# Optimization experiments

Measured on AMD Instinct MI355X. Metric: run time of the kernel, lower is better.

The kernel has to match this reference:

```python
import jax, jax.numpy as jnp
import numpy as np

N = 50000
E = 500000
C = 128
NUM_TYPES = 32
DIM_TOK = 94
STEPS = 3
BLOCKS = 2
NUM_ET = 3
LN_EPS = 1e-5


def setup_inputs() -> dict:
    key = jax.random.key(0)
    ks = jax.random.split(key, 16)
    s = 0.05
    return {
        "x_type": jax.random.randint(ks[0], (N,), 0, NUM_TYPES),
        "x_tok": jax.random.randint(ks[1], (N,), 0, DIM_TOK),
        "x_small": jax.random.normal(ks[2], (N, 2), jnp.float32),
        "edge_index": jax.random.randint(ks[3], (2, E), 0, N),
        "edge_type": jax.random.randint(ks[4], (E,), 0, NUM_ET),
        "conv_w": jax.random.normal(ks[5], (BLOCKS, NUM_ET, STEPS, C, C), jnp.float32) * s,
        "gru_wih": jax.random.normal(ks[6], (BLOCKS, NUM_ET, 3 * C, C), jnp.float32) * s,
        "gru_whh": jax.random.normal(ks[7], (BLOCKS, NUM_ET, 3 * C, C), jnp.float32) * s,
        "gru_bih": jnp.zeros((BLOCKS, NUM_ET, 3 * C), jnp.float32),
        "gru_bhh": jnp.zeros((BLOCKS, NUM_ET, 3 * C), jnp.float32),
        "ln_g": jnp.ones((BLOCKS, C), jnp.float32),
        "ln_b": jnp.zeros((BLOCKS, C), jnp.float32),
        "head_w1": jax.random.normal(ks[8], (C, C), jnp.float32) * s,
        "head_b1": jnp.zeros((C,), jnp.float32),
        "head_w2": jax.random.normal(ks[9], (2, C), jnp.float32) * s,
        "head_b2": jnp.zeros((2,), jnp.float32),
    }


def _gru_cell(x, h, wih, whh, bih, bhh):
    # torch.nn.GRUCell: gates ordered (r, z, n)
    gi = x @ wih.T + bih  # [N, 3C]
    gh = h @ whh.T + bhh
    gi_r, gi_z, gi_n = jnp.split(gi, 3, axis=-1)
    gh_r, gh_z, gh_n = jnp.split(gh, 3, axis=-1)
    r = jax.nn.sigmoid(gi_r + gh_r)
    z = jax.nn.sigmoid(gi_z + gh_z)
    n = jnp.tanh(gi_n + r * gh_n)
    return (1.0 - z) * n + z * h


def _forward(x_small, conv_w, gru_wih, gru_whh, gru_bih, gru_bhh, ln_g, ln_b,
             head_w1, head_b1, head_w2, head_b2, x_type, x_tok, edge_index, edge_type):
    # build_features: one-hot type, one-hot (clamped) token, small feats
    h_type = jax.nn.one_hot(x_type, NUM_TYPES, dtype=x_small.dtype)
    h_tok = jax.nn.one_hot(jnp.clip(x_tok, 0, DIM_TOK - 1), DIM_TOK, dtype=x_small.dtype)
    h = jnp.concatenate([h_type, h_tok, x_small], axis=1)  # [N, C]

    src, dst = edge_index[0], edge_index[1]

    for b in range(BLOCKS):
        total = jnp.zeros_like(h)
        for t in range(NUM_ET):
            # edge-type masking implemented as weighted scatter-add (sum aggr)
            em = (edge_type == t).astype(h.dtype)[:, None]  # [E, 1]
            m = h
            for s in range(STEPS):
                x = m @ conv_w[b, t, s]                     # [N, C]
                agg = jax.ops.segment_sum(x[src] * em, dst, num_segments=N)
                m = _gru_cell(agg, m,
                              gru_wih[b, t], gru_whh[b, t],
                              gru_bih[b, t], gru_bhh[b, t])
            total = total + m
        # LayerNorm(residual) + ReLU; dropout=0 (eval)
        hr = h + total
        mu = jnp.mean(hr, axis=-1, keepdims=True)
        var = jnp.var(hr, axis=-1, keepdims=True)
        h = (hr - mu) * jax.lax.rsqrt(var + LN_EPS) * ln_g[b] + ln_b[b]
        h = jax.nn.relu(h)

    # head applied per-node (module returns head(h), not head(pooled))
    z = jax.nn.relu(h @ head_w1.T + head_b1)
    return z @ head_w2.T + head_b2  # [N, 2]


def reference(x_type, x_tok, x_small, edge_index, edge_type, conv_w, gru_wih, gru_whh,
              gru_bih, gru_bhh, ln_g, ln_b, head_w1, head_b1, head_w2, head_b2):
    return _forward(x_small, conv_w, gru_wih, gru_whh, gru_bih, gru_bhh, ln_g, ln_b,
                    head_w1, head_b1, head_w2, head_b2, x_type, x_tok, edge_index, edge_type)
```

## Files before the change

kernel.cpp:

```cpp
#include <hip/hip_runtime.h>
#include <cstdint>
#include <cstddef>

#define N_NODES 50000
#define N_EDGES 500000
#define NB 782
#define NT 150000
#define NCHUNK2 586
#define FS 49152
#define PSTR 136
#define MAXOFF 12799744u

typedef _Float16 half8 __attribute__((ext_vector_type(8)));
typedef _Float16 half2v __attribute__((ext_vector_type(2)));
typedef float floatx4 __attribute__((ext_vector_type(4)));

__device__ __forceinline__ float sigmoid_(float x) { return 1.f / (1.f + __expf(-x)); }
__device__ __forceinline__ float tanh_(float x) {
  float t = __expf(-2.f * fabsf(x));
  float r = (1.f - t) / (1.f + t);
  return copysignf(r, x);
}

__global__ __launch_bounds__(256) void k_features(_Float16* __restrict__ h,
    const int* __restrict__ xtype, const int* __restrict__ xtok,
    const float* __restrict__ xs) {
  int idx = blockIdx.x * 256 + threadIdx.x;
  if (idx >= N_NODES * 128) return;
  int n = idx >> 7, c = idx & 127;
  float v;
  if (c < 32) {
    v = (xtype[n] == c) ? 1.f : 0.f;
  } else if (c < 126) {
    int tk = xtok[n];
    tk = tk < 0 ? 0 : (tk > 93 ? 93 : tk);
    v = (tk == (c - 32)) ? 1.f : 0.f;
  } else {
    v = xs[n * 2 + (c - 126)];
  }
  h[idx] = (_Float16)v;
}

__global__ __launch_bounds__(256) void k_hist(const int* __restrict__ ei,
    const int* __restrict__ et, int* __restrict__ counts) {
  int e = blockIdx.x * 256 + threadIdx.x;
  if (e >= N_EDGES) return;
  int d = ei[N_EDGES + e];
  int ty = et[e] & 3;
  if ((unsigned)d < N_NODES && ty < 3) atomicAdd(&counts[ty * N_NODES + d], 1);
}

__global__ __launch_bounds__(256) void k_scan_a(const int* __restrict__ counts,
    int* __restrict__ bsum) {
  int i = blockIdx.x * 256 + threadIdx.x;
  int v = (i < NT) ? counts[i] : 0;
  int lane = threadIdx.x & 63, wv = threadIdx.x >> 6;
#pragma unroll
  for (int off = 32; off > 0; off >>= 1) v += __shfl_xor(v, off);
  __shared__ int ws[4];
  if (lane == 0) ws[wv] = v;
  __syncthreads();
  if (threadIdx.x == 0) bsum[blockIdx.x] = ws[0] + ws[1] + ws[2] + ws[3];
}

__global__ __launch_bounds__(256) void k_scan_b(const int* __restrict__ bsum,
    int* __restrict__ boff) {
  __shared__ int ws[4];
  __shared__ int run_s;
  if (threadIdx.x == 0) run_s = 0;
  __syncthreads();
  int lane = threadIdx.x & 63, wv = threadIdx.x >> 6;
  for (int base = 0; base < NCHUNK2; base += 256) {
    int i = base + threadIdx.x;
    int v = (i < NCHUNK2) ? bsum[i] : 0;
    int s = v;
#pragma unroll
    for (int off = 1; off < 64; off <<= 1) { int u = __shfl_up(s, off); if (lane >= off) s += u; }
    if (lane == 63) ws[wv] = s;
    __syncthreads();
    int woff = 0;
#pragma unroll
    for (int w = 0; w < 4; ++w) woff += (w < wv) ? ws[w] : 0;
    int run = run_s;
    if (i < NCHUNK2) boff[i] = run + woff + s - v;
    __syncthreads();
    if (threadIdx.x == 255) run_s = run + woff + s;
    __syncthreads();
  }
  if (threadIdx.x == 0) boff[NCHUNK2] = run_s;
}

__global__ __launch_bounds__(256) void k_scan_c(const int* __restrict__ counts,
    const int* __restrict__ boff, int* __restrict__ ptr, int* __restrict__ fill) {
  int i = blockIdx.x * 256 + threadIdx.x;
  int v = (i < NT) ? counts[i] : 0;
  int lane = threadIdx.x & 63, wv = threadIdx.x >> 6;
  int s = v;
#pragma unroll
  for (int off = 1; off < 64; off <<= 1) { int u = __shfl_up(s, off); if (lane >= off) s += u; }
  __shared__ int ws[4];
  if (lane == 63) ws[wv] = s;
  __syncthreads();
  int woff = 0;
#pragma unroll
  for (int w = 0; w < 4; ++w) woff += (w < wv) ? ws[w] : 0;
  int excl = boff[blockIdx.x] + woff + s - v;
  if (i < NT) { ptr[i] = excl; fill[i] = excl; }
  if (blockIdx.x == 0 && threadIdx.x == 0) ptr[NT] = boff[NCHUNK2];
}

__global__ __launch_bounds__(256) void k_place(const int* __restrict__ ei,
    const int* __restrict__ et, int* __restrict__ fill, int* __restrict__ csr) {
  int e = blockIdx.x * 256 + threadIdx.x;
  if (e >= N_EDGES) return;
  int srcv = ei[e], d = ei[N_EDGES + e], ty = et[e] & 3;
  if ((unsigned)d >= N_NODES || (unsigned)srcv >= N_NODES || ty >= 3) return;
  int pos = atomicAdd(&fill[ty * N_NODES + d], 1);
  if ((unsigned)pos < N_EDGES) csr[pos] = srcv << 8;
}

#define PREP_A (18 * 4 * 24 * 512)
#define PREP_B (6 * 4 * 24 * 512)
__global__ __launch_bounds__(256) void k_prep_all(const float* __restrict__ cw,
    const float* __restrict__ wih, const float* __restrict__ whh,
    const float* __restrict__ hw1, _Float16* __restrict__ dcomb,
    _Float16* __restrict__ dwhh, _Float16* __restrict__ dw1) {
  int idx0 = blockIdx.x * 256 + threadIdx.x;
  if (idx0 < PREP_A) {
    int idx = idx0;
    int j = idx & 7, lane = (idx >> 3) & 63;
    int r = idx >> 9;
    int ct = r % 24;
    int r2 = r / 24;
    int kc = r2 & 3, mat = r2 >> 2;
    int bt = mat / 3;
    int k = kc * 32 + ((lane >> 4) & 3) * 8 + j;
    int n = ct * 16 + (lane & 15);
    const float* wrow = cw + ((size_t)mat * 128 + k) * 128;
    const float* irow = wih + ((size_t)bt * 384 + n) * 128;
    float acc = 0.f;
#pragma unroll
    for (int q = 0; q < 128; q += 4) {
      floatx4 a = *(const floatx4*)(wrow + q);
      floatx4 b = *(const floatx4*)(irow + q);
      acc += a[0] * b[0] + a[1] * b[1] + a[2] * b[2] + a[3] * b[3];
    }
    dcomb[idx] = (_Float16)acc;
  } else if (idx0 < PREP_A + PREP_B) {
    int idx = idx0 - PREP_A;
    int j = idx & 7, lane = (idx >> 3) & 63;
    int r = idx >> 9;
    int ct = r % 24;
    int r2 = r / 24;
    int kc = r2 & 3, bt = r2 >> 2;
    int k = kc * 32 + ((lane >> 4) & 3) * 8 + j;
    int n = ct * 16 + (lane & 15);
    dwhh[idx] = (_Float16)whh[((size_t)bt * 384 + n) * 128 + k];
  } else if (idx0 < PREP_A + PREP_B + 16384) {
    int idx = idx0 - PREP_A - PREP_B;
    int j = idx & 7, lane = (idx >> 3) & 63, ct = (idx >> 9) & 7, kc = (idx >> 12) & 3;
    int k = kc * 32 + ((lane >> 4) & 3) * 8 + j;
    int n = ct * 16 + (lane & 15);
    dw1[idx] = (_Float16)hw1[n * 128 + k];
  }
}

__global__ __launch_bounds__(512, 4) void k_step(
    const _Float16* __restrict__ Mbase, const size_t mstride,
    _Float16* __restrict__ Sout,
    const int* __restrict__ ptr, const int* __restrict__ csr,
    const _Float16* __restrict__ WPC, const _Float16* __restrict__ WHH,
    const float* __restrict__ bi2, const float* __restrict__ bh2) {
  __shared__ __attribute__((aligned(16))) _Float16 Plds[64 * PSTR];
  __shared__ __attribute__((aligned(16))) _Float16 Mlds[64 * PSTR];
  int bid = blockIdx.x;
  int t = bid / NB, blk = bid - t * NB;
  int tid = threadIdx.x;
  int wave = tid >> 6, lane = tid & 63;
  int quad = lane >> 4, l16 = lane & 15;
  int rowbase = blk * 64;
  const size_t NC = (size_t)N_NODES * 128;
  const _Float16* Mp = Mbase + mstride * t;
  const char* Mb = (const char*)Mp;
  _Float16* Sp = Sout + (size_t)t * NC;

#pragma unroll
  for (int it = 0; it < 2; ++it) {
    int r = it * 32 + (tid >> 4);
    int c = (tid & 15) * 8;
    int gr = rowbase + r; if (gr >= N_NODES) gr = N_NODES - 1;
    half8 v = *(const half8*)(Mp + (size_t)gr * 128 + c);
    *(half8*)(&Mlds[r * PSTR + c]) = v;
  }

  const int* ptrT = ptr + t * N_NODES;
  int g = quad;
  int coff = l16 * 16;
  int nlA = wave * 8 + g, nlB = nlA + 4;
  int nA = rowbase + nlA, nB = rowbase + nlB;
  int iA = 0, eA = 0, iB = 0, eB = 0;
  if (nA < N_NODES) { iA = ptrT[nA]; eA = ptrT[nA + 1]; }
  if (nB < N_NODES) { iB = ptrT[nB]; eB = ptrT[nB + 1]; }
  if (iA < 0) iA = 0; if (eA > N_EDGES) eA = N_EDGES;
  if (iB < 0) iB = 0; if (eB > N_EDGES) eB = N_EDGES;
  half8 accA = {}, accB = {};
  for (;;) {
    bool a0 = iA < eA, a1 = iA + 1 < eA;
    bool c0 = iB < eB, c1 = iB + 1 < eB;
    if (!__any(a0 || c0)) break;
    if (a0) {
      unsigned off = (unsigned)csr[iA];
      if (off > MAXOFF) off = 0;
      accA += *(const half8*)(Mb + off + coff);
    }
    if (c0) {
      unsigned off = (unsigned)csr[iB];
      if (off > MAXOFF) off = 0;
      accB += *(const half8*)(Mb + off + coff);
    }
    if (a1) {
      unsigned off = (unsigned)csr[iA + 1];
      if (off > MAXOFF) off = 0;
      accA += *(const half8*)(Mb + off + coff);
    }
    if (c1) {
      unsigned off = (unsigned)csr[iB + 1];
      if (off > MAXOFF) off = 0;
      accB += *(const half8*)(Mb + off + coff);
    }
    iA += 2; iB += 2;
  }
  *(half8*)(&Plds[nlA * PSTR + l16 * 8]) = accA;
  *(half8*)(&Plds[nlB * PSTR + l16 * 8]) = accB;
  __syncthreads();

  const half8* wpc = (const half8*)(WPC + (size_t)t * 3 * FS);
  const half8* whh = (const half8*)(WHH + (size_t)t * FS);
  const float* bi = bi2 + (size_t)t * 384;
  const float* bh = bh2 + (size_t)t * 384;
  int u = wave;
  floatx4 zero = {0.f, 0.f, 0.f, 0.f};
  floatx4 aR[4], aZ[4], aNP[4], aNM[4];
#pragma unroll
  for (int rt = 0; rt < 4; ++rt) { aR[rt] = zero; aZ[rt] = zero; aNP[rt] = zero; aNM[rt] = zero; }
#pragma unroll
  for (int kc = 0; kc < 4; ++kc) {
    half8 af[4];
#pragma unroll
    for (int rt = 0; rt < 4; ++rt)
      af[rt] = *(const half8*)(&Plds[(rt * 16 + l16) * PSTR + kc * 32 + quad * 8]);
    half8 br = wpc[(kc * 24 + u) * 64 + lane];
    half8 bz = wpc[(kc * 24 + 8 + u) * 64 + lane];
    half8 bn = wpc[(kc * 24 + 16 + u) * 64 + lane];
#pragma unroll
    for (int rt = 0; rt < 4; ++rt) {
      aR[rt] = __builtin_amdgcn_mfma_f32_16x16x32_f16(af[rt], br, aR[rt], 0, 0, 0);
      aZ[rt] = __builtin_amdgcn_mfma_f32_16x16x32_f16(af[rt], bz, aZ[rt], 0, 0, 0);
      aNP[rt] = __builtin_amdgcn_mfma_f32_16x16x32_f16(af[rt], bn, aNP[rt], 0, 0, 0);
    }
  }
#pragma unroll
  for (int kc = 0; kc < 4; ++kc) {
    half8 af[4];
#pragma unroll
    for (int rt = 0; rt < 4; ++rt)
      af[rt] = *(const half8*)(&Mlds[(rt * 16 + l16) * PSTR + kc * 32 + quad * 8]);
    half8 br = whh[(kc * 24 + u) * 64 + lane];
    half8 bz = whh[(kc * 24 + 8 + u) * 64 + lane];
    half8 bn = whh[(kc * 24 + 16 + u) * 64 + lane];
#pragma unroll
    for (int rt = 0; rt < 4; ++rt) {
      aR[rt] = __builtin_amdgcn_mfma_f32_16x16x32_f16(af[rt], br, aR[rt], 0, 0, 0);
      aZ[rt] = __builtin_amdgcn_mfma_f32_16x16x32_f16(af[rt], bz, aZ[rt], 0, 0, 0);
      aNM[rt] = __builtin_amdgcn_mfma_f32_16x16x32_f16(af[rt], bn, aNM[rt], 0, 0, 0);
    }
  }
  int col = u * 16 + l16;
  float br_ = bi[col] + bh[col];
  float bz_ = bi[128 + col] + bh[128 + col];
  float bin = bi[256 + col], bhn = bh[256 + col];
#pragma unroll
  for (int rt = 0; rt < 4; ++rt) {
#pragma unroll
    for (int q = 0; q < 4; ++q) {
      int lr = rt * 16 + quad * 4 + q;
      int row = rowbase + lr;
      if (row < N_NODES) {
        float r = sigmoid_(aR[rt][q] + br_);
        float z = sigmoid_(aZ[rt][q] + bz_);
        float nt = tanh_(aNP[rt][q] + bin + r * (aNM[rt][q] + bhn));
        float hold = (float)Mlds[lr * PSTR + col];
        Sp[(size_t)row * 128 + col] = (_Float16)((1.f - z) * nt + z * hold);
      }
    }
  }
}

__global__ __launch_bounds__(256) void k_ln(_Float16* __restrict__ h,
    const _Float16* __restrict__ S, const float* __restrict__ gamma,
    const float* __restrict__ beta) {
  int wave = threadIdx.x >> 6, lane = threadIdx.x & 63;
  int n = blockIdx.x * 4 + wave;
  if (n >= N_NODES) return;
  const size_t NC = (size_t)N_NODES * 128;
  size_t base = (size_t)n * 128 + lane * 2;
  half2v hv = *(const half2v*)(h + base);
  half2v s0 = *(const half2v*)(S + base);
  half2v s1 = *(const half2v*)(S + NC + base);
  half2v s2 = *(const half2v*)(S + 2 * NC + base);
  float v0 = (float)hv[0] + (float)s0[0] + (float)s1[0] + (float)s2[0];
  float v1 = (float)hv[1] + (float)s0[1] + (float)s1[1] + (float)s2[1];
  float s = v0 + v1, sq = v0 * v0 + v1 * v1;
#pragma unroll
  for (int off = 32; off > 0; off >>= 1) {
    s += __shfl_xor(s, off);
    sq += __shfl_xor(sq, off);
  }
  float mu = s * 0.0078125f;
  float var = sq * 0.0078125f - mu * mu;
  float rs = rsqrtf(var + 1e-5f);
  float o0 = (v0 - mu) * rs * gamma[lane * 2] + beta[lane * 2];
  float o1 = (v1 - mu) * rs * gamma[lane * 2 + 1] + beta[lane * 2 + 1];
  half2v ov; ov[0] = (_Float16)fmaxf(o0, 0.f); ov[1] = (_Float16)fmaxf(o1, 0.f);
  *(half2v*)(h + base) = ov;
}

__global__ __launch_bounds__(256, 4) void k_head(const _Float16* __restrict__ A,
    const _Float16* __restrict__ Wf, const float* __restrict__ bias,
    const float* __restrict__ w2, const float* __restrict__ b2,
    float* __restrict__ out) {
  __shared__ __attribute__((aligned(16))) _Float16 zl[64 * PSTR];
  __shared__ float w2s[256];
  int blk = blockIdx.x;
  int wave = threadIdx.x >> 6, lane = threadIdx.x & 63;
  int quad = lane >> 4, l16 = lane & 15;
  int rowbase = blk * 64;
  if (threadIdx.x < 256) w2s[threadIdx.x] = w2[threadIdx.x];
  const half8* wf = (const half8*)Wf;
  int ar[4];
#pragma unroll
  for (int rt = 0; rt < 4; ++rt) {
    int r = rowbase + rt * 16 + l16;
    ar[rt] = r < N_NODES ? r : N_NODES - 1;
  }
  floatx4 zero = {0.f, 0.f, 0.f, 0.f};
  floatx4 acc[4][2];
#pragma unroll
  for (int rt = 0; rt < 4; ++rt) { acc[rt][0] = zero; acc[rt][1] = zero; }
#pragma unroll
  for (int kc = 0; kc < 4; ++kc) {
    half8 af[4];
#pragma unroll
    for (int rt = 0; rt < 4; ++rt)
      af[rt] = *(const half8*)(A + (size_t)ar[rt] * 128 + kc * 32 + quad * 8);
    half8 b0 = wf[(kc * 8 + 2 * wave) * 64 + lane];
    half8 b1 = wf[(kc * 8 + 2 * wave + 1) * 64 + lane];
#pragma unroll
    for (int rt = 0; rt < 4; ++rt) {
      acc[rt][0] = __builtin_amdgcn_mfma_f32_16x16x32_f16(af[rt], b0, acc[rt][0], 0, 0, 0);
      acc[rt][1] = __builtin_amdgcn_mfma_f32_16x16x32_f16(af[rt], b1, acc[rt][1], 0, 0, 0);
    }
  }
  int col = wave * 32 + l16;
#pragma unroll
  for (int rt = 0; rt < 4; ++rt) {
#pragma unroll
    for (int q = 0; q < 4; ++q) {
      int lr = rt * 16 + quad * 4 + q;
      zl[lr * PSTR + col] = (_Float16)fmaxf(acc[rt][0][q] + bias[col], 0.f);
      zl[lr * PSTR + col + 16] = (_Float16)fmaxf(acc[rt][1][q] + bias[col + 16], 0.f);
    }
  }
  __syncthreads();
  int tid = threadIdx.x;
  if (tid < 128) {
    int lr = tid >> 1, o = tid & 1;
    int row = rowbase + lr;
    if (row < N_NODES) {
      const float* wr = w2s + o * 128;
      float a = 0.f;
#pragma unroll
      for (int k = 0; k < 128; ++k) a += (float)zl[lr * PSTR + k] * wr[k];
      out[(size_t)row * 2 + o] = a + b2[o];
    }
  }
}

extern "C" void kernel_launch(void* const* d_in, const int* in_sizes, int n_in,
                              void* d_out, int out_size, void* d_ws, size_t ws_size,
                              hipStream_t stream) {
  const int*   x_type  = (const int*)d_in[0];
  const int*   x_tok   = (const int*)d_in[1];
  const float* x_small = (const float*)d_in[2];
  const int*   eidx    = (const int*)d_in[3];
  const int*   etype   = (const int*)d_in[4];
  const float* conv_w  = (const float*)d_in[5];
  const float* gwih    = (const float*)d_in[6];
  const float* gwhh    = (const float*)d_in[7];
  const float* gbih    = (const float*)d_in[8];
  const float* gbhh    = (const float*)d_in[9];
  const float* ln_g    = (const float*)d_in[10];
  const float* ln_b    = (const float*)d_in[11];
  const float* hw1     = (const float*)d_in[12];
  const float* hb1     = (const float*)d_in[13];
  const float* hw2     = (const float*)d_in[14];
  const float* hb2     = (const float*)d_in[15];
  float* out = (float*)d_out;

  const size_t NC = (size_t)N_NODES * 128;
  char* W = (char*)d_ws;
  size_t off = 0;
  _Float16* h16 = (_Float16*)(W + off);     off += NC * 2;
  _Float16* S0  = (_Float16*)(W + off);     off += 3 * NC * 2;
  _Float16* S1  = (_Float16*)(W + off);     off += 3 * NC * 2;
  int* counts = (int*)(W + off);            off += (size_t)NT * 4;
  int* ptrv   = (int*)(W + off);            off += (size_t)(NT + 1) * 4;
  int* fill   = (int*)(W + off);            off += (size_t)NT * 4;
  int* bsum   = (int*)(W + off);            off += (NCHUNK2 + 1) * 4;
  int* boff   = (int*)(W + off);            off += (NCHUNK2 + 1) * 4;
  int* csr    = (int*)(W + off);            off += (size_t)N_EDGES * 4;
  _Float16* WPC = (_Float16*)(W + off);     off += (size_t)18 * FS * 2;
  _Float16* WHH = (_Float16*)(W + off);     off += (size_t)6 * FS * 2;
  _Float16* W1F = (_Float16*)(W + off);     off += (size_t)16384 * 2;

  k_features<<<(N_NODES * 128 + 255) / 256, 256, 0, stream>>>(h16, x_type, x_tok, x_small);
  hipMemsetAsync(counts, 0, (size_t)NT * 4, stream);
  k_hist<<<(N_EDGES + 255) / 256, 256, 0, stream>>>(eidx, etype, counts);
  k_scan_a<<<NCHUNK2, 256, 0, stream>>>(counts, bsum);
  k_scan_b<<<1, 256, 0, stream>>>(bsum, boff);
  k_scan_c<<<NCHUNK2, 256, 0, stream>>>(counts, boff, ptrv, fill);
  k_place<<<(N_EDGES + 255) / 256, 256, 0, stream>>>(eidx, etype, fill, csr);
  k_prep_all<<<(PREP_A + PREP_B + 16384 + 255) / 256, 256, 0, stream>>>(
      conv_w, gwih, gwhh, hw1, WPC, WHH, W1F);

  for (int b = 0; b < 2; ++b) {
    for (int s = 0; s < 3; ++s) {
      const _Float16* Msrc = (s == 0) ? h16 : ((s == 1) ? S0 : S1);
      size_t mstr = (s == 0) ? 0 : NC;
      _Float16* Sout = (s == 1) ? S1 : S0;
      k_step<<<3 * NB, 512, 0, stream>>>(Msrc, mstr, Sout, ptrv, csr,
          WPC + (size_t)(b * 9 + s) * FS, WHH + (size_t)b * 3 * FS,
          gbih + (size_t)b * 3 * 384, gbhh + (size_t)b * 3 * 384);
    }
    k_ln<<<(N_NODES + 3) / 4, 256, 0, stream>>>(h16, S0, ln_g + b * 128, ln_b + b * 128);
  }
  k_head<<<NB, 256, 0, stream>>>(h16, W1F, hb1, hw2, hb2, out);
}
```

Measured before the change: 825.7 us.

## Stage per-block CSR edge lists in LDS and compute combined weights with MFMA

The step kernel now loads the block's 65 row pointers and up to 768 edge source offsets into shared memory once, then gathers neighbor rows using LDS-resident indices with a 4-way unrolled loop, falling back to global reads past the cap. The combined conv_w·W_ih weight preparation moves from a scalar per-element dot-product kernel to an MFMA-based kernel, and the remaining prep goes into a separate kernel. This aims to cut repeated global index loads and the cost of weight preprocessing. The trade-offs are extra shared memory and synchronizations per block, plus fp16 rounding of the inputs before the combined weight product.

```diff
diff --git a/kernel.cpp b/kernel.cpp
--- a/kernel.cpp
+++ b/kernel.cpp
@@ -10,6 +10,7 @@
 #define FS 49152
 #define PSTR 136
 #define MAXOFF 12799744u
+#define ECAP 768
 
 typedef _Float16 half8 __attribute__((ext_vector_type(8)));
 typedef _Float16 half2v __attribute__((ext_vector_type(2)));
@@ -119,35 +120,70 @@
   if ((unsigned)pos < N_EDGES) csr[pos] = srcv << 8;
 }
 
-#define PREP_A (18 * 4 * 24 * 512)
+
+__global__ __launch_bounds__(512) void k_prep_cmb(const float* __restrict__ cw,
+    const float* __restrict__ wih, _Float16* __restrict__ dst) {
+  int mat = blockIdx.x >> 1, half = blockIdx.x & 1;
+  int bt = mat / 3;
+  int u = threadIdx.x >> 6, lane = threadIdx.x & 63;
+  int quad = lane >> 4, l16 = lane & 15;
+  floatx4 zero = {0.f, 0.f, 0.f, 0.f};
+  floatx4 acc[4][3];
+#pragma unroll
+  for (int rt = 0; rt < 4; ++rt)
+#pragma unroll
+    for (int cc = 0; cc < 3; ++cc) acc[rt][cc] = zero;
+#pragma unroll
+  for (int jc = 0; jc < 4; ++jc) {
+    half8 af[4], bf[3];
+#pragma unroll
+    for (int rt = 0; rt < 4; ++rt) {
+      int m = half * 64 + rt * 16 + l16;
+      const float* ap = cw + ((size_t)mat * 128 + m) * 128 + jc * 32 + quad * 8;
+      floatx4 a0 = *(const floatx4*)ap;
+      floatx4 a1 = *(const floatx4*)(ap + 4);
+#pragma unroll
+      for (int i = 0; i < 4; ++i) { af[rt][i] = (_Float16)a0[i]; af[rt][4 + i] = (_Float16)a1[i]; }
+    }
+#pragma unroll
+    for (int cc = 0; cc < 3; ++cc) {
+      int n = (u * 3 + cc) * 16 + l16;
+      const float* bp = wih + ((size_t)bt * 384 + n) * 128 + jc * 32 + quad * 8;
+      floatx4 b0 = *(const floatx4*)bp;
+      floatx4 b1 = *(const floatx4*)(bp + 4);
+#pragma unroll
+      for (int i = 0; i < 4; ++i) { bf[cc][i] = (_Float16)b0[i]; bf[cc][4 + i] = (_Float16)b1[i]; }
+    }
+#pragma unroll
+    for (int rt = 0; rt < 4; ++rt)
+#pragma unroll
+      for (int cc = 0; cc < 3; ++cc)
+        acc[rt][cc] = __builtin_amdgcn_mfma_f32_16x16x32_f16(af[rt], bf[cc], acc[rt][cc], 0, 0, 0);
+  }
+#pragma unroll
+  for (int rt = 0; rt < 4; ++rt) {
+#pragma unroll
+    for (int cc = 0; cc < 3; ++cc) {
+      int ctg = u * 3 + cc;
+#pragma unroll
+      for (int q = 0; q < 4; ++q) {
+        int k = half * 64 + rt * 16 + quad * 4 + q;
+        int kc2 = k >> 5, r5 = k & 31;
+        int lane2 = (r5 >> 3) * 16 + l16, j2 = r5 & 7;
+        dst[(size_t)mat * FS + (size_t)((kc2 * 24 + ctg) * 64 + lane2) * 8 + j2] =
+            (_Float16)acc[rt][cc][q];
+      }
+    }
+  }
+}
+
 #define PREP_B (6 * 4 * 24 * 512)
-__global__ __launch_bounds__(256) void k_prep_all(const float* __restrict__ cw,
-    const float* __restrict__ wih, const float* __restrict__ whh,
-    const float* __restrict__ hw1, _Float16* __restrict__ dcomb,
-    _Float16* __restrict__ dwhh, _Float16* __restrict__ dw1) {
+__global__ __launch_bounds__(256) void k_prep_misc(const float* __restrict__ whh,
+    const float* __restrict__ hw1, _Float16* __restrict__ dwhh,
+    _Float16* __restrict__ dw1) {
   int idx0 = blockIdx.x * 256 + threadIdx.x;
-  if (idx0 < PREP_A) {
+  if (idx0 < PREP_B) {
     int idx = idx0;
-    int j = idx & 7, lane = (idx >> 3) & 63;
-    int r = idx >> 9;
-    int ct = r % 24;
-    int r2 = r / 24;
-    int kc = r2 & 3, mat = r2 >> 2;
-    int bt = mat / 3;
-    int k = kc * 32 + ((lane >> 4) & 3) * 8 + j;
-    int n = ct * 16 + (lane & 15);
-    const float* wrow = cw + ((size_t)mat * 128 + k) * 128;
-    const float* irow = wih + ((size_t)bt * 384 + n) * 128;
-    float acc = 0.f;
-#pragma unroll
-    for (int q = 0; q < 128; q += 4) {
-      floatx4 a = *(const floatx4*)(wrow + q);
-      floatx4 b = *(const floatx4*)(irow + q);
-      acc += a[0] * b[0] + a[1] * b[1] + a[2] * b[2] + a[3] * b[3];
-    }
-    dcomb[idx] = (_Float16)acc;
-  } else if (idx0 < PREP_A + PREP_B) {
-    int idx = idx0 - PREP_A;
     int j = idx & 7, lane = (idx >> 3) & 63;
     int r = idx >> 9;
     int ct = r % 24;
@@ -156,8 +192,8 @@
     int k = kc * 32 + ((lane >> 4) & 3) * 8 + j;
     int n = ct * 16 + (lane & 15);
     dwhh[idx] = (_Float16)whh[((size_t)bt * 384 + n) * 128 + k];
-  } else if (idx0 < PREP_A + PREP_B + 16384) {
-    int idx = idx0 - PREP_A - PREP_B;
+  } else if (idx0 < PREP_B + 16384) {
+    int idx = idx0 - PREP_B;
     int j = idx & 7, lane = (idx >> 3) & 63, ct = (idx >> 9) & 7, kc = (idx >> 12) & 3;
     int k = kc * 32 + ((lane >> 4) & 3) * 8 + j;
     int n = ct * 16 + (lane & 15);
@@ -173,6 +209,8 @@
     const float* __restrict__ bi2, const float* __restrict__ bh2) {
   __shared__ __attribute__((aligned(16))) _Float16 Plds[64 * PSTR];
   __shared__ __attribute__((aligned(16))) _Float16 Mlds[64 * PSTR];
+  __shared__ int Elds[ECAP];
+  __shared__ int Pt[65];
   int bid = blockIdx.x;
   int t = bid / NB, blk = bid - t * NB;
   int tid = threadIdx.x;
@@ -183,7 +221,16 @@
   const _Float16* Mp = Mbase + mstride * t;
   const char* Mb = (const char*)Mp;
   _Float16* Sp = Sout + (size_t)t * NC;
-
+  const int* ptrT = ptr + t * N_NODES;
+
+  if (tid < 65) {
+    int n = rowbase + tid;
+    if (n > N_NODES) n = N_NODES;
+    int v = ptrT[n];
+    if (v < 0) v = 0;
+    if (v > N_EDGES) v = N_EDGES;
+    Pt[tid] = v;
+  }
 #pragma unroll
   for (int it = 0; it < 2; ++it) {
     int r = it * 32 + (tid >> 4);
@@ -192,43 +239,39 @@
     half8 v = *(const half8*)(Mp + (size_t)gr * 128 + c);
     *(half8*)(&Mlds[r * PSTR + c]) = v;
   }
-
-  const int* ptrT = ptr + t * N_NODES;
+  __syncthreads();
+
+  int bse = Pt[0];
+  int cnt = Pt[64] - bse;
+  if (cnt < 0) cnt = 0;
+  for (int i = tid; i < cnt && i < ECAP; i += 512) Elds[i] = csr[bse + i];
+  __syncthreads();
+
   int g = quad;
   int coff = l16 * 16;
   int nlA = wave * 8 + g, nlB = nlA + 4;
-  int nA = rowbase + nlA, nB = rowbase + nlB;
-  int iA = 0, eA = 0, iB = 0, eB = 0;
-  if (nA < N_NODES) { iA = ptrT[nA]; eA = ptrT[nA + 1]; }
-  if (nB < N_NODES) { iB = ptrT[nB]; eB = ptrT[nB + 1]; }
-  if (iA < 0) iA = 0; if (eA > N_EDGES) eA = N_EDGES;
-  if (iB < 0) iB = 0; if (eB > N_EDGES) eB = N_EDGES;
+  int iA = Pt[nlA] - bse, eA = Pt[nlA + 1] - bse;
+  int iB = Pt[nlB] - bse, eB = Pt[nlB + 1] - bse;
+  if (iA < 0) iA = 0; if (eA > cnt) eA = cnt; if (eA < iA) eA = iA;
+  if (iB < 0) iB = 0; if (eB > cnt) eB = cnt; if (eB < iB) eB = iB;
   half8 accA = {}, accB = {};
-  for (;;) {
-    bool a0 = iA < eA, a1 = iA + 1 < eA;
-    bool c0 = iB < eB, c1 = iB + 1 < eB;
-    if (!__any(a0 || c0)) break;
-    if (a0) {
-      unsigned off = (unsigned)csr[iA];
-      if (off > MAXOFF) off = 0;
-      accA += *(const half8*)(Mb + off + coff);
-    }
-    if (c0) {
-      unsigned off = (unsigned)csr[iB];
-      if (off > MAXOFF) off = 0;
-      accB += *(const half8*)(Mb + off + coff);
-    }
-    if (a1) {
-      unsigned off = (unsigned)csr[iA + 1];
-      if (off > MAXOFF) off = 0;
-      accA += *(const half8*)(Mb + off + coff);
-    }
-    if (c1) {
-      unsigned off = (unsigned)csr[iB + 1];
-      if (off > MAXOFF) off = 0;
-      accB += *(const half8*)(Mb + off + coff);
-    }
-    iA += 2; iB += 2;
+  while (__any(iA < eA || iB < eB)) {
+#pragma unroll
+    for (int uu = 0; uu < 4; ++uu) {
+      if (iA + uu < eA) {
+        int ii = iA + uu;
+        unsigned off = (unsigned)((ii < ECAP) ? Elds[ii] : csr[bse + ii]);
+        if (off > MAXOFF) off = 0;
+        accA += *(const half8*)(Mb + off + coff);
+      }
+      if (iB + uu < eB) {
+        int ii = iB + uu;
+        unsigned off = (unsigned)((ii < ECAP) ? Elds[ii] : csr[bse + ii]);
+        if (off > MAXOFF) off = 0;
+        accB += *(const half8*)(Mb + off + coff);
+      }
+    }
+    iA += 4; iB += 4;
   }
   *(half8*)(&Plds[nlA * PSTR + l16 * 8]) = accA;
   *(half8*)(&Plds[nlB * PSTR + l16 * 8]) = accB;
@@ -430,8 +473,8 @@
   k_scan_b<<<1, 256, 0, stream>>>(bsum, boff);
   k_scan_c<<<NCHUNK2, 256, 0, stream>>>(counts, boff, ptrv, fill);
   k_place<<<(N_EDGES + 255) / 256, 256, 0, stream>>>(eidx, etype, fill, csr);
-  k_prep_all<<<(PREP_A + PREP_B + 16384 + 255) / 256, 256, 0, stream>>>(
-      conv_w, gwih, gwhh, hw1, WPC, WHH, W1F);
+  k_prep_cmb<<<36, 512, 0, stream>>>(conv_w, gwih, WPC);
+  k_prep_misc<<<(PREP_B + 16384 + 255) / 256, 256, 0, stream>>>(gwhh, hw1, WHH, W1F);
 
   for (int b = 0; b < 2; ++b) {
     for (int s = 0; s < 3; ++s) {
```

New measurement: 724.2 us. -12.3%, faster.
